# Kernel optimization log

Measured on AMD Instinct MI355X. Metric: run time of the kernel, lower is better.

## Reference

```python
import jax, jax.numpy as jnp
import numpy as np

BETA = 0.25
GAMMA = 0.9
EPS = 1e-05
B, H, W, D, K = 64, 32, 32, 256, 1024


def setup_inputs() -> dict:
    key = jax.random.key(0)
    k1, k2 = jax.random.split(key)
    return {
        "inputs": jax.random.normal(k1, (B, H, W, D), dtype=jnp.float32),
        "codebook": jax.random.normal(k2, (D, K), dtype=jnp.float32),
        "ema_hidden_cluster": jnp.zeros((K,), dtype=jnp.float32),
        "ema_hidden_dw": jnp.zeros((D, K), dtype=jnp.float32),
        "counter": 1,  # counter after increment (fresh state: 0 + 1)
    }


def reference(inputs, codebook, ema_hidden_cluster, ema_hidden_dw, counter):
    d, k = codebook.shape
    flat = inputs.reshape(-1, d)  # [N, D]
    distances = (
        jnp.sum(jnp.square(flat), 1, keepdims=True)
        - 2.0 * jnp.matmul(flat, codebook)
        + jnp.sum(jnp.square(codebook), 0, keepdims=True)
    )
    encoding_indices = jnp.argmin(distances, axis=1)  # [N]
    encodings = jax.nn.one_hot(encoding_indices, k, dtype=distances.dtype)  # [N, K]
    flat_quantized = jnp.take(codebook, encoding_indices, axis=1).swapaxes(1, 0)  # [N, D]
    quantized = flat_quantized.reshape(inputs.shape)
    loss = BETA * jnp.mean(jnp.square(jax.lax.stop_gradient(quantized) - inputs))

    # --- EMA codebook update (training=True path) ---
    decay = jnp.float32(GAMMA)
    one = jnp.float32(1.0)
    bias = one - jnp.power(decay, counter)
    cluster_size = jnp.sum(encodings, axis=0)  # [K]
    hid_cs = ema_hidden_cluster * decay + cluster_size * (one - decay)
    avg_cs = hid_cs / bias
    dw = jnp.matmul(flat.T, encodings)  # [D, K]
    hid_dw = ema_hidden_dw * decay + dw * (one - decay)
    avg_dw = hid_dw / bias
    n = jnp.sum(avg_cs)
    smoothed_cs = (avg_cs + EPS) / (n + k * EPS) * n
    new_codebook = avg_dw / smoothed_cs[None, :]

    ste = inputs + jax.lax.stop_gradient(quantized - inputs)
    avg_probs = jnp.mean(encodings, 0)
    perplexity = jnp.exp(-jnp.sum(avg_probs * jnp.log(avg_probs + 1e-10)))
    return (ste, perplexity, loss, new_codebook)
```

## Files before the change

### kernel.cpp

```cpp
#include <hip/hip_runtime.h>

#define N 65536
#define D 256
#define K 1024
#define BETA 0.25f
#define GAMMA 0.9f
#define EPS 1e-5f

#define QBLOCKS 512
#define DWROWS 64

#define OFF_INDICES 0
#define OFF_PERM    262144
#define OFF_COUNTS  524288
#define OFF_CNORM   528384
#define OFF_OFFSETS 532480
#define OFF_CURSOR  536576
#define OFF_SMOOTH  540672
#define OFF_LOSSP   544768
#define OFF_CBT     546816
#define OFF_CBE     1595392

typedef __bf16 bf16x8 __attribute__((ext_vector_type(8)));
typedef short  s16x8  __attribute__((ext_vector_type(8)));
typedef float  f32x4  __attribute__((ext_vector_type(4)));

__device__ inline unsigned short f32_to_bf16_rn(float f) {
    unsigned int u = __float_as_uint(f);
    unsigned int r = u + 0x7fffu + ((u >> 16) & 1u);
    return (unsigned short)(r >> 16);
}

__device__ inline f32x4 mfma16(s16x8 a, s16x8 b, f32x4 c) {
    return __builtin_amdgcn_mfma_f32_16x16x32_bf16(
        __builtin_bit_cast(bf16x8, a), __builtin_bit_cast(bf16x8, b), c, 0, 0, 0);
}

__device__ __forceinline__ void stage16(const s16x8* __restrict__ g, s16x8* l) {
    __builtin_amdgcn_global_load_lds(
        (const __attribute__((address_space(1))) void*)g,
        (__attribute__((address_space(3))) void*)l, 16, 0, 0);
}

__global__ __launch_bounds__(256) void pack_cb(const float* __restrict__ cb,
                                               float* __restrict__ cbT,
                                               s16x8* __restrict__ cbEp,
                                               float* __restrict__ cnorm) {
    const int ct = blockIdx.x >> 2;
    const int c2 = blockIdx.x & 3;
#pragma unroll
    for (int it = 0; it < 2; ++it) {
        int u = it * 256 + threadIdx.x;
        int frgc = u >> 7;
        int ks = (u >> 6) & 1;
        int L = u & 63;
        int c = ct * 64 + frgc * 16 + (L & 15);
        int d0 = c2 * 64 + (ks * 4 + (L >> 4)) * 8;
        float v[8];
        s16x8 hv, lv;
        float ss = 0.f;
#pragma unroll
        for (int j = 0; j < 8; ++j) {
            float f = cb[(size_t)(d0 + j) * K + c];
            v[j] = f;
            unsigned short h = f32_to_bf16_rn(f);
            hv[j] = (short)h;
            lv[j] = (short)f32_to_bf16_rn(f - __uint_as_float((unsigned)h << 16));
            ss = fmaf(f, f, ss);
        }
        *(float4*)&cbT[(size_t)c * D + d0]     = make_float4(v[0], v[1], v[2], v[3]);
        *(float4*)&cbT[(size_t)c * D + d0 + 4] = make_float4(v[4], v[5], v[6], v[7]);
        cbEp[(size_t)(ct * 8 + c2) * 512 + u]     = hv;
        cbEp[(size_t)(ct * 8 + 4 + c2) * 512 + u] = lv;
        atomicAdd(&cnorm[c], ss);
    }
}

__global__ __launch_bounds__(256, 2) void argmin_mfma_kernel(
        const float* __restrict__ x,
        const s16x8* __restrict__ cbEp,
        const float* __restrict__ cnorm,
        int* __restrict__ indices) {
    __shared__ s16x8 Bs[2][1024];

    const int tid = threadIdx.x;
    const int lane = tid & 63;
    const int w = tid >> 6;
    const int r0 = blockIdx.x * 128;
    const int row16 = lane & 15;
    const int quad = lane >> 4;

#pragma unroll
    for (int i = 0; i < 4; ++i)
        stage16(cbEp + i * 256 + tid, &Bs[0][i * 256 + w * 64]);

    s16x8 Ah[2][8], Al[2][8];
#pragma unroll
    for (int frg = 0; frg < 2; ++frg) {
#pragma unroll
        for (int kb8 = 0; kb8 < 8; ++kb8) {
            const float* src = &x[(size_t)(r0 + w * 32 + frg * 16 + row16) * D
                                  + kb8 * 32 + quad * 8];
            float4 v0 = *(const float4*)src;
            float4 v1 = *(const float4*)(src + 4);
            float f[8] = {v0.x, v0.y, v0.z, v0.w, v1.x, v1.y, v1.z, v1.w};
            s16x8 hv, lv;
#pragma unroll
            for (int j = 0; j < 8; ++j) {
                unsigned short h = f32_to_bf16_rn(f[j]);
                hv[j] = (short)h;
                lv[j] = (short)f32_to_bf16_rn(f[j] - __uint_as_float((unsigned)h << 16));
            }
            Ah[frg][kb8] = hv;
            Al[frg][kb8] = lv;
        }
    }

    float minv[2][4];
    int   mini[2][4];
#pragma unroll
    for (int frg = 0; frg < 2; ++frg)
#pragma unroll
        for (int reg = 0; reg < 4; ++reg) { minv[frg][reg] = 3.4e38f; mini[frg][reg] = 0; }

    for (int ct = 0; ct < 16; ++ct) {
        f32x4 acc[2][4];
#pragma unroll
        for (int frg = 0; frg < 2; ++frg)
#pragma unroll
            for (int fc = 0; fc < 4; ++fc) acc[frg][fc] = (f32x4){0.f, 0.f, 0.f, 0.f};

#pragma unroll
        for (int ph = 0; ph < 4; ++ph) {
            __syncthreads();
            const bool has_next = !(ct == 15 && ph == 3);
            if (has_next) {
                const int nct = (ph == 3) ? ct + 1 : ct;
                const int nph = (ph == 3) ? 0 : ph + 1;
                const size_t gb = (size_t)(nct * 8 + nph * 2) * 512;
#pragma unroll
                for (int i = 0; i < 4; ++i)
                    stage16(cbEp + gb + i * 256 + tid, &Bs[(ph + 1) & 1][i * 256 + w * 64]);
            }
#pragma unroll
            for (int half = 0; half < 2; ++half) {
                const int cchunk = ph * 2 + half;
                const int c2 = cchunk & 3;
#pragma unroll
                for (int ks = 0; ks < 2; ++ks) {
                    const int ksb = c2 * 2 + ks;
#pragma unroll
                    for (int fc = 0; fc < 4; ++fc) {
                        s16x8 b = Bs[ph & 1][half * 512 + (fc * 2 + ks) * 64 + lane];
#pragma unroll
                        for (int frg = 0; frg < 2; ++frg) {
                            acc[frg][fc] = mfma16(Ah[frg][ksb], b, acc[frg][fc]);
                            if (cchunk < 4)
                                acc[frg][fc] = mfma16(Al[frg][ksb], b, acc[frg][fc]);
                        }
                    }
                }
            }
        }
#pragma unroll
        for (int fc = 0; fc < 4; ++fc) {
            int col = ct * 64 + fc * 16 + row16;
            float cn = cnorm[col];
#pragma unroll
            for (int frg = 0; frg < 2; ++frg)
#pragma unroll
                for (int reg = 0; reg < 4; ++reg) {
                    float val = fmaf(-2.f, acc[frg][fc][reg], cn);
                    if (val < minv[frg][reg]) { minv[frg][reg] = val; mini[frg][reg] = col; }
                }
        }
    }

#pragma unroll
    for (int mask = 1; mask <= 8; mask <<= 1) {
#pragma unroll
        for (int frg = 0; frg < 2; ++frg)
#pragma unroll
            for (int reg = 0; reg < 4; ++reg) {
                float ov = __shfl_xor(minv[frg][reg], mask, 64);
                int   oi = __shfl_xor(mini[frg][reg], mask, 64);
                if (ov < minv[frg][reg] ||
                    (ov == minv[frg][reg] && oi < mini[frg][reg])) {
                    minv[frg][reg] = ov; mini[frg][reg] = oi;
                }
            }
    }
    if (row16 == 0) {
#pragma unroll
        for (int frg = 0; frg < 2; ++frg)
#pragma unroll
            for (int reg = 0; reg < 4; ++reg)
                indices[r0 + w * 32 + frg * 16 + quad * 4 + reg] = mini[frg][reg];
    }
}

__global__ __launch_bounds__(256) void quantize_kernel(const float* __restrict__ x,
                                                       const float* __restrict__ cbT,
                                                       const int* __restrict__ indices,
                                                       float* __restrict__ ste,
                                                       int* __restrict__ counts,
                                                       float* __restrict__ loss_partial,
                                                       float* __restrict__ dwT) {
    const int gid = blockIdx.x * 256 + threadIdx.x;
    if (gid < (K * D / 4))
        *(float4*)&dwT[(size_t)gid * 4] = make_float4(0.f, 0.f, 0.f, 0.f);

    const int lane = threadIdx.x & 63;
    const int wid = gid >> 6;
    const int nwaves = QBLOCKS * 4;

    float s = 0.f;
    for (int row = wid; row < N; row += nwaves) {
        const int k = indices[row];
        float4 q  = *(const float4*)&cbT[(size_t)k * D + lane * 4];
        float4 xi = *(const float4*)&x[(size_t)row * D + lane * 4];
        *(float4*)&ste[(size_t)row * D + lane * 4] = q;
        float dx = q.x - xi.x, dy = q.y - xi.y, dz = q.z - xi.z, dw = q.w - xi.w;
        s = fmaf(dx, dx, s); s = fmaf(dy, dy, s);
        s = fmaf(dz, dz, s); s = fmaf(dw, dw, s);
        if (lane == 0) atomicAdd(&counts[k], 1);
    }
#pragma unroll
    for (int off = 32; off >= 1; off >>= 1) s += __shfl_down(s, off, 64);
    __shared__ float red[4];
    if (lane == 0) red[threadIdx.x >> 6] = s;
    __syncthreads();
    if (threadIdx.x == 0)
        loss_partial[blockIdx.x] = red[0] + red[1] + red[2] + red[3];
}

__global__ __launch_bounds__(1024) void finalize_kernel(const int* __restrict__ counts,
                                                        const float* __restrict__ ema_c,
                                                        const int* __restrict__ counter,
                                                        const float* __restrict__ loss_partial,
                                                        float* __restrict__ out_perp,
                                                        float* __restrict__ out_loss,
                                                        int* __restrict__ offsets,
                                                        int* __restrict__ cursor,
                                                        float* __restrict__ smoothed) {
    const int k = threadIdx.x;
    __shared__ float fred[1024];
    __shared__ int scan[1024];
    __shared__ float nsum_s;
    __shared__ float ent_s;

    const int c = counts[k];
    const float bias = 1.0f - powf(GAMMA, (float)counter[0]);
    const float hid = fmaf(ema_c[k], GAMMA, (float)c * (1.0f - GAMMA));
    const float avg = hid / bias;

    fred[k] = avg;
    __syncthreads();
    for (int s = 512; s >= 1; s >>= 1) {
        if (k < s) fred[k] += fred[k + s];
        __syncthreads();
    }
    if (k == 0) nsum_s = fred[0];
    __syncthreads();
    const float nsum = nsum_s;

    float p = (float)c * (1.0f / (float)N);
    fred[k] = p * logf(p + 1e-10f);
    __syncthreads();
    for (int s = 512; s >= 1; s >>= 1) {
        if (k < s) fred[k] += fred[k + s];
        __syncthreads();
    }
    if (k == 0) ent_s = fred[0];
    __syncthreads();

    fred[k] = (k < QBLOCKS) ? loss_partial[k] : 0.f;
    __syncthreads();
    for (int s = 512; s >= 1; s >>= 1) {
        if (k < s) fred[k] += fred[k + s];
        __syncthreads();
    }

    scan[k] = c;
    __syncthreads();
    for (int s = 1; s < 1024; s <<= 1) {
        int v = (k >= s) ? scan[k - s] : 0;
        __syncthreads();
        scan[k] += v;
        __syncthreads();
    }
    const int excl = scan[k] - c;
    offsets[k] = excl;
    cursor[k] = excl;

    smoothed[k] = (avg + EPS) / (nsum + (float)K * EPS) * nsum;

    if (k == 0) {
        out_perp[0] = expf(-ent_s);
        out_loss[0] = BETA * fred[0] * (1.0f / ((float)N * (float)D));
    }
}

__global__ __launch_bounds__(256) void scatter_kernel(const int* __restrict__ indices,
                                                      int* __restrict__ cursor,
                                                      int* __restrict__ perm,
                                                      int* __restrict__ skey) {
    const int n = blockIdx.x * 256 + threadIdx.x;
    const int k = indices[n];
    const int pos = atomicAdd(&cursor[k], 1);
    perm[pos] = n;
    skey[pos] = k;
}

__global__ __launch_bounds__(256) void dw_accum_kernel(const float* __restrict__ x,
                                                       const int* __restrict__ perm,
                                                       const int* __restrict__ skey,
                                                       float* __restrict__ dwT) {
    __shared__ int s_rows[DWROWS];
    __shared__ int s_keys[DWROWS + 1];
    const int d = threadIdx.x;
    const int base = blockIdx.x * DWROWS;
    if (threadIdx.x < DWROWS) {
        s_rows[threadIdx.x] = perm[base + threadIdx.x];
        s_keys[threadIdx.x] = skey[base + threadIdx.x];
    }
    if (threadIdx.x == 0) s_keys[DWROWS] = -1;
    __syncthreads();
    float acc = 0.f;
#pragma unroll 4
    for (int i = 0; i < DWROWS; ++i) {
        acc += x[(size_t)s_rows[i] * D + d];
        if (s_keys[i + 1] != s_keys[i]) {
            atomicAdd(&dwT[(size_t)s_keys[i] * D + d], acc);
            acc = 0.f;
        }
    }
}

__global__ __launch_bounds__(256) void codebook_final_kernel(const float* __restrict__ dwT,
                                                             const float* __restrict__ ema_dw,
                                                             const float* __restrict__ smoothed,
                                                             const int* __restrict__ counter,
                                                             float* __restrict__ out_cb) {
    __shared__ float tile[64][65];
    const int d0 = (blockIdx.x & 3) * 64;
    const int k0 = (blockIdx.x >> 2) * 64;
    const int tid = threadIdx.x;
#pragma unroll
    for (int it = 0; it < 16; ++it) {
        int idx = it * 256 + tid;
        int kk = idx >> 6, dd = idx & 63;
        tile[kk][dd] = dwT[(size_t)(k0 + kk) * D + d0 + dd];
    }
    __syncthreads();
    const float bias = 1.0f - powf(GAMMA, (float)counter[0]);
#pragma unroll
    for (int it = 0; it < 16; ++it) {
        int idx = it * 256 + tid;
        int dd = idx >> 6, kk = idx & 63;
        float dwv = tile[kk][dd];
        float hid = fmaf(ema_dw[(size_t)(d0 + dd) * K + k0 + kk], GAMMA,
                         dwv * (1.0f - GAMMA));
        out_cb[(size_t)(d0 + dd) * K + k0 + kk] = (hid / bias) / smoothed[k0 + kk];
    }
}

extern "C" void kernel_launch(void* const* d_in, const int* in_sizes, int n_in,
                              void* d_out, int out_size, void* d_ws, size_t ws_size,
                              hipStream_t stream) {
    const float* x       = (const float*)d_in[0];
    const float* cb      = (const float*)d_in[1];
    const float* ema_c   = (const float*)d_in[2];
    const float* ema_dw  = (const float*)d_in[3];
    const int*   counter = (const int*)d_in[4];

    float* out = (float*)d_out;
    float* ste = out;
    float* out_perp = out + (size_t)N * D;
    float* out_loss = out_perp + 1;
    float* out_cb = out_perp + 2;

    char* ws = (char*)d_ws;
    int* indices  = (int*)(ws + OFF_INDICES);
    int* perm     = (int*)(ws + OFF_PERM);
    int* counts   = (int*)(ws + OFF_COUNTS);
    float* cnorm  = (float*)(ws + OFF_CNORM);
    int* offsets  = (int*)(ws + OFF_OFFSETS);
    int* cursor   = (int*)(ws + OFF_CURSOR);
    float* smooth = (float*)(ws + OFF_SMOOTH);
    float* lossp  = (float*)(ws + OFF_LOSSP);
    float* cbT    = (float*)(ws + OFF_CBT);
    s16x8* cbEp   = (s16x8*)(ws + OFF_CBE);
    int* skey     = (int*)(ws + OFF_CBT);
    float* dwT    = (float*)(ws + OFF_CBE);

    hipMemsetAsync(counts, 0, 2 * K * sizeof(int), stream);

    pack_cb<<<64, 256, 0, stream>>>(cb, cbT, cbEp, cnorm);
    argmin_mfma_kernel<<<N / 128, 256, 0, stream>>>(x, cbEp, cnorm, indices);
    quantize_kernel<<<QBLOCKS, 256, 0, stream>>>(x, cbT, indices, ste, counts, lossp, dwT);
    finalize_kernel<<<1, 1024, 0, stream>>>(counts, ema_c, counter, lossp,
                                            out_perp, out_loss, offsets, cursor, smooth);
    scatter_kernel<<<N / 256, 256, 0, stream>>>(indices, cursor, perm, skey);
    dw_accum_kernel<<<N / DWROWS, 256, 0, stream>>>(x, perm, skey, dwT);
    codebook_final_kernel<<<64, 256, 0, stream>>>(dwT, ema_dw, smooth, counter, out_cb);
}
```

Baseline: 335.2 us.

## Fuse quantize pass into dw accumulation and move counting into argmin

Removes the separate quantize kernel. Cluster counts are now accumulated with atomics in the argmin epilogue, and the STE write plus the loss partials are computed inside the dw accumulation kernel, which already reads x in sorted order. dwT zeroing moves into the scatter kernel, the perm/key arrays are packed into one int, and the loss reduction moves into codebook_final. This saves one full read of x and one kernel launch, but STE writes are now scattered rows per block, and the loss partials reuse the cnorm workspace.

```diff
diff --git a/kernel.cpp b/kernel.cpp
--- a/kernel.cpp
+++ b/kernel.cpp
@@ -7,7 +7,6 @@
 #define GAMMA 0.9f
 #define EPS 1e-5f
 
-#define QBLOCKS 512
 #define DWROWS 64
 
 #define OFF_INDICES 0
@@ -80,7 +79,8 @@
         const float* __restrict__ x,
         const s16x8* __restrict__ cbEp,
         const float* __restrict__ cnorm,
-        int* __restrict__ indices) {
+        int* __restrict__ indices,
+        int* __restrict__ counts) {
     __shared__ s16x8 Bs[2][1024];
 
     const int tid = threadIdx.x;
@@ -194,60 +194,24 @@
 #pragma unroll
         for (int frg = 0; frg < 2; ++frg)
 #pragma unroll
-            for (int reg = 0; reg < 4; ++reg)
-                indices[r0 + w * 32 + frg * 16 + quad * 4 + reg] = mini[frg][reg];
-    }
-}
-
-__global__ __launch_bounds__(256) void quantize_kernel(const float* __restrict__ x,
-                                                       const float* __restrict__ cbT,
-                                                       const int* __restrict__ indices,
-                                                       float* __restrict__ ste,
-                                                       int* __restrict__ counts,
-                                                       float* __restrict__ loss_partial,
-                                                       float* __restrict__ dwT) {
-    const int gid = blockIdx.x * 256 + threadIdx.x;
-    if (gid < (K * D / 4))
-        *(float4*)&dwT[(size_t)gid * 4] = make_float4(0.f, 0.f, 0.f, 0.f);
-
-    const int lane = threadIdx.x & 63;
-    const int wid = gid >> 6;
-    const int nwaves = QBLOCKS * 4;
-
-    float s = 0.f;
-    for (int row = wid; row < N; row += nwaves) {
-        const int k = indices[row];
-        float4 q  = *(const float4*)&cbT[(size_t)k * D + lane * 4];
-        float4 xi = *(const float4*)&x[(size_t)row * D + lane * 4];
-        *(float4*)&ste[(size_t)row * D + lane * 4] = q;
-        float dx = q.x - xi.x, dy = q.y - xi.y, dz = q.z - xi.z, dw = q.w - xi.w;
-        s = fmaf(dx, dx, s); s = fmaf(dy, dy, s);
-        s = fmaf(dz, dz, s); s = fmaf(dw, dw, s);
-        if (lane == 0) atomicAdd(&counts[k], 1);
-    }
-#pragma unroll
-    for (int off = 32; off >= 1; off >>= 1) s += __shfl_down(s, off, 64);
-    __shared__ float red[4];
-    if (lane == 0) red[threadIdx.x >> 6] = s;
-    __syncthreads();
-    if (threadIdx.x == 0)
-        loss_partial[blockIdx.x] = red[0] + red[1] + red[2] + red[3];
+            for (int reg = 0; reg < 4; ++reg) {
+                const int idx = mini[frg][reg];
+                indices[r0 + w * 32 + frg * 16 + quad * 4 + reg] = idx;
+                atomicAdd(&counts[idx], 1);
+            }
+    }
 }
 
 __global__ __launch_bounds__(1024) void finalize_kernel(const int* __restrict__ counts,
                                                         const float* __restrict__ ema_c,
                                                         const int* __restrict__ counter,
-                                                        const float* __restrict__ loss_partial,
                                                         float* __restrict__ out_perp,
-                                                        float* __restrict__ out_loss,
-                                                        int* __restrict__ offsets,
                                                         int* __restrict__ cursor,
                                                         float* __restrict__ smoothed) {
     const int k = threadIdx.x;
     __shared__ float fred[1024];
     __shared__ int scan[1024];
     __shared__ float nsum_s;
-    __shared__ float ent_s;
 
     const int c = counts[k];
     const float bias = 1.0f - powf(GAMMA, (float)counter[0]);
@@ -271,15 +235,7 @@
         if (k < s) fred[k] += fred[k + s];
         __syncthreads();
     }
-    if (k == 0) ent_s = fred[0];
-    __syncthreads();
-
-    fred[k] = (k < QBLOCKS) ? loss_partial[k] : 0.f;
-    __syncthreads();
-    for (int s = 512; s >= 1; s >>= 1) {
-        if (k < s) fred[k] += fred[k + s];
-        __syncthreads();
-    }
+    if (k == 0) out_perp[0] = expf(-fred[0]);
 
     scan[k] = c;
     __syncthreads();
@@ -289,63 +245,89 @@
         scan[k] += v;
         __syncthreads();
     }
-    const int excl = scan[k] - c;
-    offsets[k] = excl;
-    cursor[k] = excl;
+    cursor[k] = scan[k] - c;
 
     smoothed[k] = (avg + EPS) / (nsum + (float)K * EPS) * nsum;
-
-    if (k == 0) {
-        out_perp[0] = expf(-ent_s);
-        out_loss[0] = BETA * fred[0] * (1.0f / ((float)N * (float)D));
-    }
 }
 
 __global__ __launch_bounds__(256) void scatter_kernel(const int* __restrict__ indices,
                                                       int* __restrict__ cursor,
-                                                      int* __restrict__ perm,
-                                                      int* __restrict__ skey) {
+                                                      int* __restrict__ permk,
+                                                      float* __restrict__ dwT) {
     const int n = blockIdx.x * 256 + threadIdx.x;
+    *(float4*)&dwT[(size_t)n * 4] = make_float4(0.f, 0.f, 0.f, 0.f);
     const int k = indices[n];
     const int pos = atomicAdd(&cursor[k], 1);
-    perm[pos] = n;
-    skey[pos] = k;
-}
-
-__global__ __launch_bounds__(256) void dw_accum_kernel(const float* __restrict__ x,
-                                                       const int* __restrict__ perm,
-                                                       const int* __restrict__ skey,
-                                                       float* __restrict__ dwT) {
+    permk[pos] = n | (k << 16);
+}
+
+__global__ __launch_bounds__(256) void dw_fused_kernel(const float* __restrict__ x,
+                                                       const float* __restrict__ cbT,
+                                                       const int* __restrict__ permk,
+                                                       float* __restrict__ ste,
+                                                       float* __restrict__ dwT,
+                                                       float* __restrict__ lossp) {
     __shared__ int s_rows[DWROWS];
     __shared__ int s_keys[DWROWS + 1];
     const int d = threadIdx.x;
     const int base = blockIdx.x * DWROWS;
     if (threadIdx.x < DWROWS) {
-        s_rows[threadIdx.x] = perm[base + threadIdx.x];
-        s_keys[threadIdx.x] = skey[base + threadIdx.x];
+        const int pk = permk[base + threadIdx.x];
+        s_rows[threadIdx.x] = pk & 0xffff;
+        s_keys[threadIdx.x] = pk >> 16;
     }
     if (threadIdx.x == 0) s_keys[DWROWS] = -1;
     __syncthreads();
     float acc = 0.f;
+    float ls = 0.f;
 #pragma unroll 4
     for (int i = 0; i < DWROWS; ++i) {
-        acc += x[(size_t)s_rows[i] * D + d];
-        if (s_keys[i + 1] != s_keys[i]) {
-            atomicAdd(&dwT[(size_t)s_keys[i] * D + d], acc);
+        const int n = s_rows[i];
+        const int k = s_keys[i];
+        const float xv = x[(size_t)n * D + d];
+        const float q  = cbT[(size_t)k * D + d];
+        ste[(size_t)n * D + d] = q;
+        acc += xv;
+        const float df = q - xv;
+        ls = fmaf(df, df, ls);
+        if (s_keys[i + 1] != k) {
+            atomicAdd(&dwT[(size_t)k * D + d], acc);
             acc = 0.f;
         }
     }
+#pragma unroll
+    for (int off = 32; off >= 1; off >>= 1) ls += __shfl_down(ls, off, 64);
+    __shared__ float red[4];
+    if ((d & 63) == 0) red[d >> 6] = ls;
+    __syncthreads();
+    if (d == 0) lossp[blockIdx.x] = red[0] + red[1] + red[2] + red[3];
 }
 
 __global__ __launch_bounds__(256) void codebook_final_kernel(const float* __restrict__ dwT,
                                                              const float* __restrict__ ema_dw,
                                                              const float* __restrict__ smoothed,
                                                              const int* __restrict__ counter,
-                                                             float* __restrict__ out_cb) {
+                                                             const float* __restrict__ lossp,
+                                                             float* __restrict__ out_cb,
+                                                             float* __restrict__ out_loss) {
     __shared__ float tile[64][65];
+    __shared__ float lred[4];
+    const int tid = threadIdx.x;
+
+    if (blockIdx.x == 0) {
+        float s = lossp[tid] + lossp[tid + 256] + lossp[tid + 512] + lossp[tid + 768];
+#pragma unroll
+        for (int off = 32; off >= 1; off >>= 1) s += __shfl_down(s, off, 64);
+        if ((tid & 63) == 0) lred[tid >> 6] = s;
+        __syncthreads();
+        if (tid == 0)
+            out_loss[0] = BETA * (lred[0] + lred[1] + lred[2] + lred[3])
+                          * (1.0f / ((float)N * (float)D));
+        __syncthreads();
+    }
+
     const int d0 = (blockIdx.x & 3) * 64;
     const int k0 = (blockIdx.x >> 2) * 64;
-    const int tid = threadIdx.x;
 #pragma unroll
     for (int it = 0; it < 16; ++it) {
         int idx = it * 256 + tid;
@@ -382,26 +364,24 @@
 
     char* ws = (char*)d_ws;
     int* indices  = (int*)(ws + OFF_INDICES);
-    int* perm     = (int*)(ws + OFF_PERM);
+    int* permk    = (int*)(ws + OFF_PERM);
     int* counts   = (int*)(ws + OFF_COUNTS);
     float* cnorm  = (float*)(ws + OFF_CNORM);
-    int* offsets  = (int*)(ws + OFF_OFFSETS);
     int* cursor   = (int*)(ws + OFF_CURSOR);
     float* smooth = (float*)(ws + OFF_SMOOTH);
-    float* lossp  = (float*)(ws + OFF_LOSSP);
     float* cbT    = (float*)(ws + OFF_CBT);
     s16x8* cbEp   = (s16x8*)(ws + OFF_CBE);
-    int* skey     = (int*)(ws + OFF_CBT);
     float* dwT    = (float*)(ws + OFF_CBE);
+    float* lossp  = (float*)(ws + OFF_CNORM);
 
     hipMemsetAsync(counts, 0, 2 * K * sizeof(int), stream);
 
     pack_cb<<<64, 256, 0, stream>>>(cb, cbT, cbEp, cnorm);
-    argmin_mfma_kernel<<<N / 128, 256, 0, stream>>>(x, cbEp, cnorm, indices);
-    quantize_kernel<<<QBLOCKS, 256, 0, stream>>>(x, cbT, indices, ste, counts, lossp, dwT);
-    finalize_kernel<<<1, 1024, 0, stream>>>(counts, ema_c, counter, lossp,
-                                            out_perp, out_loss, offsets, cursor, smooth);
-    scatter_kernel<<<N / 256, 256, 0, stream>>>(indices, cursor, perm, skey);
-    dw_accum_kernel<<<N / DWROWS, 256, 0, stream>>>(x, perm, skey, dwT);
-    codebook_final_kernel<<<64, 256, 0, stream>>>(dwT, ema_dw, smooth, counter, out_cb);
-}
+    argmin_mfma_kernel<<<N / 128, 256, 0, stream>>>(x, cbEp, cnorm, indices, counts);
+    finalize_kernel<<<1, 1024, 0, stream>>>(counts, ema_c, counter,
+                                            out_perp, cursor, smooth);
+    scatter_kernel<<<N / 256, 256, 0, stream>>>(indices, cursor, permk, dwT);
+    dw_fused_kernel<<<N / DWROWS, 256, 0, stream>>>(x, cbT, permk, ste, dwT, lossp);
+    codebook_final_kernel<<<64, 256, 0, stream>>>(dwT, ema_dw, smooth, counter,
+                                                  lossp, out_cb, out_loss);
+}
```

New measurement: 311.2 us. 1.08x faster.
